# Performance work log

Hardware: AMD Instinct MI355X
Metric: run time of the kernel (lower is better)

The kernel has to match this reference:

```python
import jax, jax.numpy as jnp
import numpy as np

D_MODEL, D_STATE, D_CONV, EXPAND = 2048, 16, 4, 2
D_INNER = EXPAND * D_MODEL            # 4096
DT_RANK = -(-D_MODEL // 16)           # 128 (mamba default: ceil(d_model/16))
D_OUT = 1024
SEQ = 1024


def setup_inputs():
    key = jax.random.key(0)
    k = jax.random.split(key, 8)
    n = lambda ki, shp, s=0.02: (jax.random.normal(ki, shp) * s).astype(jnp.float32)
    return {
        "input_param": jax.random.normal(k[0], (1, SEQ, D_MODEL), dtype=jnp.float32),  # nn.init.normal_, std=1
        "in_proj_w": n(k[1], (2 * D_INNER, D_MODEL)),
        "conv_w": n(k[2], (D_INNER, D_CONV), 0.1),       # depthwise causal conv kernel
        "conv_b": jnp.zeros((D_INNER,), jnp.float32),
        "x_proj_w": n(k[3], (DT_RANK + 2 * D_STATE, D_INNER)),
        "dt_proj_w": n(k[4], (D_INNER, DT_RANK), 0.1),
        "dt_proj_b": jnp.full((D_INNER,), -4.0, jnp.float32),  # softplus(-4) ~ small dt
        "A_log": jnp.log(jnp.broadcast_to(jnp.arange(1, D_STATE + 1, dtype=jnp.float32), (D_INNER, D_STATE))),  # S4D-real init
        "D_skip": jnp.ones((D_INNER,), jnp.float32),
        "out_proj_w": n(k[5], (D_MODEL, D_INNER)),
        "out_w": n(k[6], (D_OUT, D_MODEL)),
        "out_b": jnp.zeros((D_OUT,), jnp.float32),
        "batch": 2,
    }


def _mamba_model(input_param, in_proj_w, conv_w, conv_b, x_proj_w, dt_proj_w,
                 dt_proj_b, A_log, D_skip, out_proj_w, out_w, out_b, batch):
    # learned input, repeated across batch: (B, L, d_model)
    x = jnp.broadcast_to(input_param, (batch, SEQ, D_MODEL))
    # in_proj -> x-branch and gate z, each (B, L, d_inner)
    xz = x @ in_proj_w.T
    xs, z = jnp.split(xz, 2, axis=-1)
    # causal depthwise conv1d along time (kernel D_CONV, truncated to L)
    xt = jnp.pad(xs.swapaxes(1, 2), ((0, 0), (0, 0), (D_CONV - 1, 0)))  # (B, d_inner, L+pad)
    xc = sum(conv_w[:, i][None, :, None] * xt[:, :, i:i + SEQ] for i in range(D_CONV))
    xc = xc + conv_b[None, :, None]
    u = jax.nn.silu(xc.swapaxes(1, 2))                                  # (B, L, d_inner)
    # data-dependent dt / B / C
    dbc = u @ x_proj_w.T                                                # (B, L, dt_rank + 2*d_state)
    dt, Bm, Cm = jnp.split(dbc, [DT_RANK, DT_RANK + D_STATE], axis=-1)
    delta = jax.nn.softplus(dt @ dt_proj_w.T + dt_proj_b)               # (B, L, d_inner)
    A = -jnp.exp(A_log)                                                 # (d_inner, d_state)

    # selective scan: h_t = exp(dt_t*A) h_{t-1} + dt_t*B_t*u_t ; y_t = C_t . h_t
    def step(h, inp):
        d_t, b_t, c_t, u_t = inp                     # (B,d_inner),(B,d_state),(B,d_state),(B,d_inner)
        h = jnp.exp(d_t[..., None] * A) * h + (d_t * u_t)[..., None] * b_t[:, None, :]
        return h, jnp.einsum('bds,bs->bd', h, c_t)

    h0 = jnp.zeros((batch, D_INNER, D_STATE), jnp.float32)
    _, ys = jax.lax.scan(step, h0, (delta.swapaxes(0, 1), Bm.swapaxes(0, 1),
                                    Cm.swapaxes(0, 1), u.swapaxes(0, 1)))
    y = ys.swapaxes(0, 1) + u * D_skip               # skip connection D*u
    y = y * jax.nn.silu(z)                           # gated output
    out = y @ out_proj_w.T                           # (B, L, d_model)
    return out @ out_w.T + out_b                     # to_out: (B, L, d_output)


def reference(input_param, in_proj_w, conv_w, conv_b, x_proj_w, dt_proj_w,
              dt_proj_b, A_log, D_skip, out_proj_w, out_w, out_b, batch):
    return _mamba_model(input_param, in_proj_w, conv_w, conv_b, x_proj_w, dt_proj_w,
                        dt_proj_b, A_log, D_skip, out_proj_w, out_w, out_b, batch)
```

## Files before the change

kernel.cpp:

```cpp
#include <hip/hip_runtime.h>
#include <hip/hip_bf16.h>
#include <math.h>


#define SEQ     1024
#define DMODEL  2048
#define DINNER  4096
#define DSTATE  16
#define DTRANK  128
#define DOUT    1024
#define DBC_W   (DTRANK + 2*DSTATE)

#define XP_CHUNKS 16
#define XP_KC     (DINNER / XP_CHUNKS)

#define NCHUNK  32
#define CL      (SEQ / NCHUNK)

typedef __attribute__((ext_vector_type(4))) float  f32x4;
typedef __attribute__((ext_vector_type(8))) short  bf16x8;
typedef __attribute__((ext_vector_type(8))) unsigned short u16x8;
typedef unsigned short ushort_t;

#define B_XS    ((size_t)0)
#define B_ZB    ((size_t)16777216)
#define B_U     ((size_t)25165824)
#define B_DBC   ((size_t)41943040)
#define B_DELTA ((size_t)42598400)
#define B_YGB   ((size_t)59375616)
#define B_XB    ((size_t)67764224)
#define B_WIN   ((size_t)71958528)
#define B_WOP   (B_WIN)
#define B_WOW   (B_WIN + 16777216)
#define B_PART  (B_XS)
#define B_HLOC   (B_XS)
#define B_HSTART (B_XS + 8388608)
#define B_SUMD   (B_WIN + 16777216 + 4194304)

__device__ __forceinline__ float sigf(float x) { return 1.0f / (1.0f + __expf(-x)); }
__device__ __forceinline__ ushort_t f2b(float x) {
    __hip_bfloat16 h = __float2bfloat16(x);
    return *(ushort_t*)&h;
}
__device__ __forceinline__ float b2f(ushort_t u) {
    unsigned int x = ((unsigned int)u) << 16;
    return __uint_as_float(x);
}
__device__ __forceinline__ void gload_lds16(const void* g, void* l) {
    __builtin_amdgcn_global_load_lds((const __attribute__((address_space(1))) void*)g,
                                     (__attribute__((address_space(3))) void*)l, 16, 0, 0);
}

__global__ __launch_bounds__(256) void f32_to_bf16(const float* __restrict__ in,
                                                   ushort_t* __restrict__ out, int n8) {
    int i = blockIdx.x * 256 + threadIdx.x;
    if (i >= n8) return;
    const float4* p = (const float4*)in + (size_t)i * 2;
    float4 a = p[0], b = p[1];
    u16x8 v;
    v[0] = f2b(a.x); v[1] = f2b(a.y); v[2] = f2b(a.z); v[3] = f2b(a.w);
    v[4] = f2b(b.x); v[5] = f2b(b.y); v[6] = f2b(b.z); v[7] = f2b(b.w);
    *((u16x8*)out + i) = v;
}

enum { MEPI_SPLIT_XZ = 0, MEPI_BF16 = 1, MEPI_BIAS_DUP = 2 };

template <int EPI>
__global__ __launch_bounds__(256) void gemm_mfma(
    const ushort_t* __restrict__ A,
    const ushort_t* __restrict__ W,
    int K, int N,
    float* __restrict__ C0,
    ushort_t* __restrict__ C1,
    const float* __restrict__ bias,
    float* __restrict__ C2)
{
    __shared__ __align__(16) ushort_t As[128 * 64];
    __shared__ __align__(16) ushort_t Bs[128 * 64];

    const int t    = threadIdx.x;
    const int lane = t & 63;
    const int w    = t >> 6;
    const int bm   = blockIdx.y * 128;
    const int bn   = blockIdx.x * 128;
    const int wr   = (w >> 1) * 64;
    const int wc   = (w & 1) * 64;
    const int fr   = lane & 15;
    const int g    = lane >> 4;

    f32x4 acc[4][4];
    #pragma unroll
    for (int i = 0; i < 4; i++)
        #pragma unroll
        for (int j = 0; j < 4; j++) acc[i][j] = (f32x4)0.f;

    int srow[4], sseg[4];
    #pragma unroll
    for (int i = 0; i < 4; i++) {
        int c = i * 256 + t;
        srow[i] = c >> 3;
        sseg[i] = (c & 7) ^ (srow[i] & 7);
    }

    for (int k0 = 0; k0 < K; k0 += 64) {
        #pragma unroll
        for (int i = 0; i < 4; i++) {
            const ushort_t* ga = A + (size_t)(bm + srow[i]) * K + k0 + sseg[i] * 8;
            gload_lds16(ga, &As[(i * 256 + w * 64) * 8]);
        }
        #pragma unroll
        for (int i = 0; i < 4; i++) {
            const ushort_t* gb = W + (size_t)(bn + srow[i]) * K + k0 + sseg[i] * 8;
            gload_lds16(gb, &Bs[(i * 256 + w * 64) * 8]);
        }
        __syncthreads();

        #pragma unroll
        for (int kk = 0; kk < 2; kk++) {
            bf16x8 af[4], bf[4];
            #pragma unroll
            for (int fm = 0; fm < 4; fm++) {
                int row = wr + fm * 16 + fr;
                af[fm] = *(const bf16x8*)&As[row * 64 + (((kk << 2) + g) ^ (row & 7)) * 8];
            }
            #pragma unroll
            for (int fn = 0; fn < 4; fn++) {
                int row = wc + fn * 16 + fr;
                bf[fn] = *(const bf16x8*)&Bs[row * 64 + (((kk << 2) + g) ^ (row & 7)) * 8];
            }
            #pragma unroll
            for (int fm = 0; fm < 4; fm++)
                #pragma unroll
                for (int fn = 0; fn < 4; fn++)
                    acc[fm][fn] = __builtin_amdgcn_mfma_f32_16x16x32_bf16(
                        af[fm], bf[fn], acc[fm][fn], 0, 0, 0);
        }
        __syncthreads();
    }

    #pragma unroll
    for (int fm = 0; fm < 4; fm++) {
        #pragma unroll
        for (int fn = 0; fn < 4; fn++) {
            f32x4 v = acc[fm][fn];
            int col = bn + wc + fn * 16 + fr;
            #pragma unroll
            for (int j = 0; j < 4; j++) {
                int row = bm + wr + fm * 16 + g * 4 + j;
                float x = v[j];
                if (EPI == MEPI_SPLIT_XZ) {
                    if (col < DINNER) C0[(size_t)row * DINNER + col] = x;
                    else              C1[(size_t)row * DINNER + (col - DINNER)] = f2b(x);
                } else if (EPI == MEPI_BF16) {
                    C1[(size_t)row * N + col] = f2b(x);
                } else {
                    float y = x + bias[col];
                    C0[(size_t)row * N + col] = y;
                    C2[(size_t)row * N + col] = y;
                }
            }
        }
    }
}

__global__ __launch_bounds__(256) void xproj_split(
    const float* __restrict__ U,
    const float* __restrict__ W,
    float* __restrict__ part)
{
    __shared__ float sU[16][64];
    __shared__ float sW[160][17];

    const int chunk = blockIdx.x;
    const int bm    = blockIdx.y * 64;
    const int t     = threadIdx.x;
    const int mg    = t >> 4;
    const int nt    = t & 15;

    const int k0base = chunk * XP_KC;

    float acc[4][10];
    #pragma unroll
    for (int i = 0; i < 4; i++)
        #pragma unroll
        for (int j = 0; j < 10; j++) acc[i][j] = 0.f;

    const int lrow = t >> 2;
    const int lk4  = (t & 3) * 4;

    for (int kc = 0; kc < XP_KC; kc += 16) {
        const int k0 = k0base + kc;
        float4 uv = *(const float4*)&U[(size_t)(bm + lrow) * DINNER + k0 + lk4];
        sU[lk4 + 0][lrow] = uv.x; sU[lk4 + 1][lrow] = uv.y;
        sU[lk4 + 2][lrow] = uv.z; sU[lk4 + 3][lrow] = uv.w;
        #pragma unroll
        for (int q = 0; q < 10; q++) {
            int idx = q * 256 + t;
            int n = idx >> 4, k = idx & 15;
            sW[n][k] = W[(size_t)n * DINNER + k0 + k];
        }
        __syncthreads();
        #pragma unroll
        for (int k = 0; k < 16; k++) {
            float4 a4 = *(const float4*)&sU[k][mg * 4];
            const float ar[4] = {a4.x, a4.y, a4.z, a4.w};
            #pragma unroll
            for (int j = 0; j < 10; j++) {
                float b = sW[nt + 16 * j][k];
                #pragma unroll
                for (int i = 0; i < 4; i++)
                    acc[i][j] = fmaf(ar[i], b, acc[i][j]);
            }
        }
        __syncthreads();
    }

    float* pout = part + ((size_t)chunk * SEQ + bm) * 160;
    #pragma unroll
    for (int i = 0; i < 4; i++) {
        int row = mg * 4 + i;
        #pragma unroll
        for (int j = 0; j < 10; j++)
            pout[(size_t)row * 160 + nt + 16 * j] = acc[i][j];
    }
}

__global__ __launch_bounds__(256) void xproj_reduce(
    const float* __restrict__ part, float* __restrict__ dbc)
{
    int i = blockIdx.x * 256 + threadIdx.x;
    if (i >= SEQ * 160) return;
    float s = 0.f;
    #pragma unroll
    for (int c = 0; c < XP_CHUNKS; c++) s += part[(size_t)c * (SEQ * 160) + i];
    dbc[i] = s;
}

enum { EPI_NONE = 0, EPI_SOFTPLUS = 1 };

template <int EPI>
__global__ __launch_bounds__(256) void gemm_nt(
    const float* __restrict__ A, int lda,
    const float* __restrict__ W,
    float* __restrict__ C, int ldc,
    int M, int N, int K,
    const float* __restrict__ bias)
{
    __shared__ float As[16][64];
    __shared__ float Ws[16][64];

    const int bm = blockIdx.y * 64;
    const int bn = blockIdx.x * 64;
    const int t  = threadIdx.x;
    const int tx = t & 15;
    const int ty = t >> 4;
    const int lr  = t >> 2;
    const int lc4 = (t & 3) * 4;

    float acc[4][4] = {{0.f,0.f,0.f,0.f},{0.f,0.f,0.f,0.f},{0.f,0.f,0.f,0.f},{0.f,0.f,0.f,0.f}};

    const bool aval = (bm + lr) < M;
    const bool wval = (bn + lr) < N;
    const float* Aptr = A + (size_t)(bm + lr) * lda + lc4;
    const float* Wptr = W + (size_t)(bn + lr) * K + lc4;

    for (int k0 = 0; k0 < K; k0 += 16) {
        float4 av = make_float4(0.f, 0.f, 0.f, 0.f);
        float4 wv = make_float4(0.f, 0.f, 0.f, 0.f);
        if (aval) av = *(const float4*)(Aptr + k0);
        if (wval) wv = *(const float4*)(Wptr + k0);
        As[lc4 + 0][lr] = av.x; As[lc4 + 1][lr] = av.y;
        As[lc4 + 2][lr] = av.z; As[lc4 + 3][lr] = av.w;
        Ws[lc4 + 0][lr] = wv.x; Ws[lc4 + 1][lr] = wv.y;
        Ws[lc4 + 2][lr] = wv.z; Ws[lc4 + 3][lr] = wv.w;
        __syncthreads();
        #pragma unroll
        for (int k = 0; k < 16; k++) {
            float4 a4 = *(const float4*)&As[k][ty * 4];
            float4 b4 = *(const float4*)&Ws[k][tx * 4];
            const float ar[4] = {a4.x, a4.y, a4.z, a4.w};
            const float br[4] = {b4.x, b4.y, b4.z, b4.w};
            #pragma unroll
            for (int i = 0; i < 4; i++)
                #pragma unroll
                for (int j = 0; j < 4; j++)
                    acc[i][j] = fmaf(ar[i], br[j], acc[i][j]);
        }
        __syncthreads();
    }

    #pragma unroll
    for (int i = 0; i < 4; i++) {
        int gm = bm + ty * 4 + i;
        if (gm >= M) continue;
        #pragma unroll
        for (int j = 0; j < 4; j++) {
            int gn = bn + tx * 4 + j;
            if (gn >= N) continue;
            float v = acc[i][j];
            if (EPI == EPI_SOFTPLUS) {
                v += bias[gn];
                v = (v > 20.f) ? v : log1pf(__expf(v));
            }
            C[(size_t)gm * ldc + gn] = v;
        }
    }
}

__global__ __launch_bounds__(256) void conv_silu_kernel(
    const float* __restrict__ xs,
    const float* __restrict__ conv_w,
    const float* __restrict__ conv_b,
    float* __restrict__ u)
{
    int idx = blockIdx.x * 256 + threadIdx.x;
    if (idx >= SEQ * DINNER) return;
    int d = idx & (DINNER - 1);
    int tt = idx >> 12;
    float acc = conv_b[d];
    #pragma unroll
    for (int i = 0; i < 4; i++) {
        int ts = tt - 3 + i;
        if (ts >= 0) acc = fmaf(conv_w[d * 4 + i], xs[(size_t)ts * DINNER + d], acc);
    }
    u[idx] = acc * sigf(acc);
}

__global__ __launch_bounds__(256) void scan_pass1(
    const float* __restrict__ delta,
    const float* __restrict__ u,
    const float* __restrict__ dbc,
    const float* __restrict__ A_log,
    float* __restrict__ Hloc,
    float* __restrict__ SumD)
{
    const int d     = blockIdx.x * 256 + threadIdx.x;
    const int chunk = blockIdx.y;
    const int t0    = chunk * CL;

    __shared__ float sB[CL][16];
    #pragma unroll
    for (int q = 0; q < (CL * 16) / 256; q++) {
        int idx = q * 256 + threadIdx.x;
        int i = idx >> 4, j = idx & 15;
        sB[i][j] = dbc[(size_t)(t0 + i) * DBC_W + DTRANK + j];
    }
    __syncthreads();

    float A_[16];
    #pragma unroll
    for (int s = 0; s < 16; s++) A_[s] = -__expf(A_log[(size_t)d * DSTATE + s]);

    float h[16];
    #pragma unroll
    for (int s = 0; s < 16; s++) h[s] = 0.f;
    float sum = 0.f;

    float dl = delta[(size_t)t0 * DINNER + d];
    float uu = u[(size_t)t0 * DINNER + d];
    for (int i = 0; i < CL; i++) {
        float dln = 0.f, uun = 0.f;
        if (i + 1 < CL) {
            dln = delta[(size_t)(t0 + i + 1) * DINNER + d];
            uun = u[(size_t)(t0 + i + 1) * DINNER + d];
        }
        float du = dl * uu;
        sum += dl;
        #pragma unroll
        for (int s = 0; s < 16; s++)
            h[s] = fmaf(__expf(dl * A_[s]), h[s], du * sB[i][s]);
        dl = dln; uu = uun;
    }

    float4* hp = (float4*)&Hloc[((size_t)chunk * DINNER + d) * DSTATE];
    #pragma unroll
    for (int q = 0; q < 4; q++)
        hp[q] = make_float4(h[q * 4], h[q * 4 + 1], h[q * 4 + 2], h[q * 4 + 3]);
    SumD[(size_t)chunk * DINNER + d] = sum;
}

__global__ __launch_bounds__(256) void scan_combine(
    const float* __restrict__ Hloc,
    const float* __restrict__ SumD,
    const float* __restrict__ A_log,
    float* __restrict__ Hstart)
{
    int idx = blockIdx.x * 256 + threadIdx.x;
    int d = idx >> 4;
    const float Acoef = -__expf(A_log[idx]);
    float Hs = 0.f;
    #pragma unroll
    for (int c = 0; c < NCHUNK; c++) {
        Hstart[(size_t)c * (DINNER * DSTATE) + idx] = Hs;
        Hs = fmaf(__expf(Acoef * SumD[(size_t)c * DINNER + d]), Hs,
                  Hloc[(size_t)c * (DINNER * DSTATE) + idx]);
    }
}

__global__ __launch_bounds__(256) void scan_pass2(
    const float* __restrict__ delta,
    const float* __restrict__ u,
    const float* __restrict__ dbc,
    const float* __restrict__ A_log,
    const float* __restrict__ D_skip,
    const ushort_t* __restrict__ zb,
    const float* __restrict__ Hstart,
    ushort_t* __restrict__ ygb)
{
    const int d     = blockIdx.x * 256 + threadIdx.x;
    const int chunk = blockIdx.y;
    const int t0    = chunk * CL;

    __shared__ float sB[CL][16];
    __shared__ float sC[CL][16];
    #pragma unroll
    for (int q = 0; q < (CL * 16) / 256; q++) {
        int idx = q * 256 + threadIdx.x;
        int i = idx >> 4, j = idx & 15;
        sB[i][j] = dbc[(size_t)(t0 + i) * DBC_W + DTRANK + j];
        sC[i][j] = dbc[(size_t)(t0 + i) * DBC_W + DTRANK + DSTATE + j];
    }
    __syncthreads();

    float A_[16];
    #pragma unroll
    for (int s = 0; s < 16; s++) A_[s] = -__expf(A_log[(size_t)d * DSTATE + s]);

    float h[16];
    const float4* hp = (const float4*)&Hstart[((size_t)chunk * DINNER + d) * DSTATE];
    #pragma unroll
    for (int q = 0; q < 4; q++) {
        float4 v = hp[q];
        h[q * 4] = v.x; h[q * 4 + 1] = v.y; h[q * 4 + 2] = v.z; h[q * 4 + 3] = v.w;
    }

    const float Dsk = D_skip[d];

    float dl = delta[(size_t)t0 * DINNER + d];
    float uu = u[(size_t)t0 * DINNER + d];
    for (int i = 0; i < CL; i++) {
        float dln = 0.f, uun = 0.f;
        if (i + 1 < CL) {
            dln = delta[(size_t)(t0 + i + 1) * DINNER + d];
            uun = u[(size_t)(t0 + i + 1) * DINNER + d];
        }
        float du = dl * uu;
        float y = 0.f;
        #pragma unroll
        for (int s = 0; s < 16; s++) {
            h[s] = fmaf(__expf(dl * A_[s]), h[s], du * sB[i][s]);
            y = fmaf(h[s], sC[i][s], y);
        }
        float yv = y + uu * Dsk;
        float z = b2f(zb[(size_t)(t0 + i) * DINNER + d]);
        yv *= z * sigf(z);
        ygb[(size_t)(t0 + i) * DINNER + d] = f2b(yv);
        dl = dln; uu = uun;
    }
}

extern "C" void kernel_launch(void* const* d_in, const int* in_sizes, int n_in,
                              void* d_out, int out_size, void* d_ws, size_t ws_size,
                              hipStream_t stream)
{
    const float* input_param = (const float*)d_in[0];
    const float* in_proj_w   = (const float*)d_in[1];
    const float* conv_w      = (const float*)d_in[2];
    const float* conv_b      = (const float*)d_in[3];
    const float* x_proj_w    = (const float*)d_in[4];
    const float* dt_proj_w   = (const float*)d_in[5];
    const float* dt_proj_b   = (const float*)d_in[6];
    const float* A_log       = (const float*)d_in[7];
    const float* D_skip      = (const float*)d_in[8];
    const float* out_proj_w  = (const float*)d_in[9];
    const float* out_w       = (const float*)d_in[10];
    const float* out_b       = (const float*)d_in[11];

    char* ws = (char*)d_ws;
    float*    XS     = (float*)(ws + B_XS);
    ushort_t* ZB     = (ushort_t*)(ws + B_ZB);
    float*    U      = (float*)(ws + B_U);
    float*    DBC    = (float*)(ws + B_DBC);
    float*    DELTA  = (float*)(ws + B_DELTA);
    ushort_t* YGB    = (ushort_t*)(ws + B_YGB);
    ushort_t* XB     = (ushort_t*)(ws + B_XB);
    ushort_t* OB     = (ushort_t*)(ws + B_XB);
    ushort_t* WINB   = (ushort_t*)(ws + B_WIN);
    ushort_t* WOPB   = (ushort_t*)(ws + B_WOP);
    ushort_t* WOWB   = (ushort_t*)(ws + B_WOW);
    float*    PART   = (float*)(ws + B_PART);
    float*    HLOC   = (float*)(ws + B_HLOC);
    float*    HSTART = (float*)(ws + B_HSTART);
    float*    SUMD   = (float*)(ws + B_SUMD);

    float* out = (float*)d_out;

    f32_to_bf16<<<dim3((SEQ * DMODEL / 8) / 256), 256, 0, stream>>>(input_param, XB, SEQ * DMODEL / 8);
    f32_to_bf16<<<dim3((2 * DINNER * DMODEL / 8) / 256), 256, 0, stream>>>(in_proj_w, WINB, 2 * DINNER * DMODEL / 8);

    gemm_mfma<MEPI_SPLIT_XZ><<<dim3(2 * DINNER / 128, SEQ / 128), 256, 0, stream>>>(
        XB, WINB, DMODEL, 2 * DINNER, XS, ZB, nullptr, nullptr);

    f32_to_bf16<<<dim3((DMODEL * DINNER / 8) / 256), 256, 0, stream>>>(out_proj_w, WOPB, DMODEL * DINNER / 8);
    f32_to_bf16<<<dim3((DOUT * DMODEL / 8) / 256), 256, 0, stream>>>(out_w, WOWB, DOUT * DMODEL / 8);

    conv_silu_kernel<<<dim3(SEQ * DINNER / 256), 256, 0, stream>>>(XS, conv_w, conv_b, U);

    xproj_split<<<dim3(XP_CHUNKS, SEQ / 64), 256, 0, stream>>>(U, x_proj_w, PART);
    xproj_reduce<<<dim3(SEQ * 160 / 256), 256, 0, stream>>>(PART, DBC);

    gemm_nt<EPI_SOFTPLUS><<<dim3(DINNER / 64, SEQ / 64), 256, 0, stream>>>(
        DBC, DBC_W, dt_proj_w, DELTA, DINNER, SEQ, DINNER, DTRANK, dt_proj_b);

    scan_pass1<<<dim3(DINNER / 256, NCHUNK), 256, 0, stream>>>(
        DELTA, U, DBC, A_log, HLOC, SUMD);
    scan_combine<<<dim3(DINNER * DSTATE / 256), 256, 0, stream>>>(
        HLOC, SUMD, A_log, HSTART);
    scan_pass2<<<dim3(DINNER / 256, NCHUNK), 256, 0, stream>>>(
        DELTA, U, DBC, A_log, D_skip, ZB, HSTART, YGB);

    gemm_mfma<MEPI_BF16><<<dim3(DMODEL / 128, SEQ / 128), 256, 0, stream>>>(
        YGB, WOPB, DINNER, DMODEL, nullptr, OB, nullptr, nullptr);

    gemm_mfma<MEPI_BIAS_DUP><<<dim3(DOUT / 128, SEQ / 128), 256, 0, stream>>>(
        OB, WOWB, DMODEL, DOUT, out, nullptr, out_b, out + (size_t)SEQ * DOUT);
}
```

Before: 463.5 us.

## Split-K the out_proj and to_out GEMMs with separate reduction kernels

The two final GEMMs (1024x2048x4096 and 1024x1024x2048) launched only 128 and 64 blocks on a GPU with 256 CUs, leaving most of the device idle. They now split K four ways via gridDim.z, write fp32 partials to workspace, and reduce them in new elementwise kernels that also apply bf16 conversion or bias plus the duplicated output. This adds partial-sum memory traffic and two extra launches in exchange for higher occupancy.

```diff
diff --git a/kernel.cpp b/kernel.cpp
--- a/kernel.cpp
+++ b/kernel.cpp
@@ -17,9 +17,12 @@
 #define NCHUNK  32
 #define CL      (SEQ / NCHUNK)
 
+#define GSPLIT  4
+
 typedef __attribute__((ext_vector_type(4))) float  f32x4;
 typedef __attribute__((ext_vector_type(8))) short  bf16x8;
 typedef __attribute__((ext_vector_type(8))) unsigned short u16x8;
+typedef __attribute__((ext_vector_type(4))) unsigned short u16x4;
 typedef unsigned short ushort_t;
 
 #define B_XS    ((size_t)0)
@@ -36,6 +39,7 @@
 #define B_HLOC   (B_XS)
 #define B_HSTART (B_XS + 8388608)
 #define B_SUMD   (B_WIN + 16777216 + 4194304)
+#define B_GP     (B_XS)
 
 __device__ __forceinline__ float sigf(float x) { return 1.0f / (1.0f + __expf(-x)); }
 __device__ __forceinline__ ushort_t f2b(float x) {
@@ -63,7 +67,7 @@
     *((u16x8*)out + i) = v;
 }
 
-enum { MEPI_SPLIT_XZ = 0, MEPI_BF16 = 1, MEPI_BIAS_DUP = 2 };
+enum { MEPI_SPLIT_XZ = 0, MEPI_BF16 = 1, MEPI_BIAS_DUP = 2, MEPI_PARTIAL = 3 };
 
 template <int EPI>
 __global__ __launch_bounds__(256) void gemm_mfma(
@@ -102,7 +106,11 @@
         sseg[i] = (c & 7) ^ (srow[i] & 7);
     }
 
-    for (int k0 = 0; k0 < K; k0 += 64) {
+    const int Kc   = K / gridDim.z;
+    const int kbeg = blockIdx.z * Kc;
+    const int kend = kbeg + Kc;
+
+    for (int k0 = kbeg; k0 < kend; k0 += 64) {
         #pragma unroll
         for (int i = 0; i < 4; i++) {
             const ushort_t* ga = A + (size_t)(bm + srow[i]) * K + k0 + sseg[i] * 8;
@@ -138,6 +146,7 @@
         __syncthreads();
     }
 
+    const int M = gridDim.y * 128;
     #pragma unroll
     for (int fm = 0; fm < 4; fm++) {
         #pragma unroll
@@ -153,14 +162,53 @@
                     else              C1[(size_t)row * DINNER + (col - DINNER)] = f2b(x);
                 } else if (EPI == MEPI_BF16) {
                     C1[(size_t)row * N + col] = f2b(x);
-                } else {
+                } else if (EPI == MEPI_BIAS_DUP) {
                     float y = x + bias[col];
                     C0[(size_t)row * N + col] = y;
                     C2[(size_t)row * N + col] = y;
+                } else {
+                    C0[(size_t)blockIdx.z * M * N + (size_t)row * N + col] = x;
                 }
             }
         }
     }
+}
+
+__global__ __launch_bounds__(256) void reduce4_bf16(
+    const float* __restrict__ part, ushort_t* __restrict__ ob, int n4)
+{
+    int i = blockIdx.x * 256 + threadIdx.x;
+    if (i >= n4) return;
+    const float4* p = (const float4*)part;
+    float4 s = p[i];
+    #pragma unroll
+    for (int c = 1; c < GSPLIT; c++) {
+        float4 a = p[(size_t)c * n4 + i];
+        s.x += a.x; s.y += a.y; s.z += a.z; s.w += a.w;
+    }
+    u16x4 v;
+    v[0] = f2b(s.x); v[1] = f2b(s.y); v[2] = f2b(s.z); v[3] = f2b(s.w);
+    *((u16x4*)ob + i) = v;
+}
+
+__global__ __launch_bounds__(256) void reduce4_bias_dup(
+    const float* __restrict__ part, const float* __restrict__ bias,
+    float* __restrict__ o0, float* __restrict__ o1, int n4)
+{
+    int i = blockIdx.x * 256 + threadIdx.x;
+    if (i >= n4) return;
+    const float4* p = (const float4*)part;
+    float4 s = p[i];
+    #pragma unroll
+    for (int c = 1; c < GSPLIT; c++) {
+        float4 a = p[(size_t)c * n4 + i];
+        s.x += a.x; s.y += a.y; s.z += a.z; s.w += a.w;
+    }
+    int col0 = (i * 4) & (DOUT - 1);
+    float4 b = *(const float4*)&bias[col0];
+    s.x += b.x; s.y += b.y; s.z += b.z; s.w += b.w;
+    ((float4*)o0)[i] = s;
+    ((float4*)o1)[i] = s;
 }
 
 __global__ __launch_bounds__(256) void xproj_split(
@@ -492,6 +540,7 @@
     float*    HLOC   = (float*)(ws + B_HLOC);
     float*    HSTART = (float*)(ws + B_HSTART);
     float*    SUMD   = (float*)(ws + B_SUMD);
+    float*    GP     = (float*)(ws + B_GP);
 
     float* out = (float*)d_out;
 
@@ -519,9 +568,12 @@
     scan_pass2<<<dim3(DINNER / 256, NCHUNK), 256, 0, stream>>>(
         DELTA, U, DBC, A_log, D_skip, ZB, HSTART, YGB);
 
-    gemm_mfma<MEPI_BF16><<<dim3(DMODEL / 128, SEQ / 128), 256, 0, stream>>>(
-        YGB, WOPB, DINNER, DMODEL, nullptr, OB, nullptr, nullptr);
-
-    gemm_mfma<MEPI_BIAS_DUP><<<dim3(DOUT / 128, SEQ / 128), 256, 0, stream>>>(
-        OB, WOWB, DMODEL, DOUT, out, nullptr, out_b, out + (size_t)SEQ * DOUT);
-}
+    gemm_mfma<MEPI_PARTIAL><<<dim3(DMODEL / 128, SEQ / 128, GSPLIT), 256, 0, stream>>>(
+        YGB, WOPB, DINNER, DMODEL, GP, nullptr, nullptr, nullptr);
+    reduce4_bf16<<<dim3((SEQ * DMODEL / 4) / 256), 256, 0, stream>>>(GP, OB, SEQ * DMODEL / 4);
+
+    gemm_mfma<MEPI_PARTIAL><<<dim3(DOUT / 128, SEQ / 128, GSPLIT), 256, 0, stream>>>(
+        OB, WOWB, DMODEL, DOUT, GP, nullptr, nullptr, nullptr);
+    reduce4_bias_dup<<<dim3((SEQ * DOUT / 4) / 256), 256, 0, stream>>>(
+        GP, out_b, out, out + (size_t)SEQ * DOUT, SEQ * DOUT / 4);
+}
```

New measurement: 410.5 us. -11.4%, faster.
